# Kernel tuning notes

Measured on AMD Instinct MI355X. Metric: run time of the kernel, lower is better.

The kernel has to match this reference:

```python
import jax, jax.numpy as jnp
import numpy as np

N = 33_554_432  # 2^25 elements
N_CLASSES = 6


def setup_inputs() -> dict:
    key = jax.random.key(0)
    k1, k2 = jax.random.split(key)
    inputs = jax.random.normal(k1, (N,), dtype=jnp.float32)
    # targets are integer class labels stored as float32 (as torch l1_loss expects floats)
    targets = jax.random.randint(k2, (N,), 0, N_CLASSES).astype(jnp.float32)
    return {"inputs": inputs, "targets": targets}


def reference(inputs, targets):
    # Single-pass segment reduction replacing the per-class masked-gather loop.
    seg = targets.astype(jnp.int32)                      # class id per element
    absdiff = jnp.abs(inputs - targets)                  # |pred - target|
    sums = jax.ops.segment_sum(absdiff, seg, num_segments=N_CLASSES)
    counts = jax.ops.segment_sum(jnp.ones_like(absdiff), seg, num_segments=N_CLASSES)
    # Classes with zero members contribute 0 (the torch loop skips them).
    per_class_mae = jnp.where(counts > 0, sums / jnp.maximum(counts, 1.0), 0.0)
    return jnp.sum(per_class_mae) / N_CLASSES
```

## Files before the change

### kernel.cpp

```cpp
#include <hip/hip_runtime.h>

#define NCLASSES 6

__device__ __forceinline__ float wave_reduce_sum(float v) {
#pragma unroll
    for (int off = 32; off > 0; off >>= 1)
        v += __shfl_down(v, off, 64);
    return v;
}

__global__ void __launch_bounds__(256)
mae_partial_kernel(const float* __restrict__ inputs,
                   const float* __restrict__ targets,
                   float* __restrict__ partials,
                   int n) {
    float sums[NCLASSES] = {0.f, 0.f, 0.f, 0.f, 0.f, 0.f};
    float cnts[NCLASSES] = {0.f, 0.f, 0.f, 0.f, 0.f, 0.f};

    const int tid = blockIdx.x * blockDim.x + threadIdx.x;
    const int nthreads = gridDim.x * blockDim.x;
    const int n4 = n >> 2;

    const float4* __restrict__ in4 = reinterpret_cast<const float4*>(inputs);
    const float4* __restrict__ tg4 = reinterpret_cast<const float4*>(targets);

    for (int i = tid; i < n4; i += nthreads) {
        float4 x = in4[i];
        float4 t = tg4[i];

        float xs[4] = {x.x, x.y, x.z, x.w};
        float ts[4] = {t.x, t.y, t.z, t.w};
#pragma unroll
        for (int j = 0; j < 4; ++j) {
            float ad = fabsf(xs[j] - ts[j]);
#pragma unroll
            for (int k = 0; k < NCLASSES; ++k) {
                bool m = (ts[j] == (float)k);
                sums[k] += m ? ad : 0.f;
                cnts[k] += m ? 1.f : 0.f;
            }
        }
    }

    const int tail_start = n4 << 2;
    for (int i = tail_start + tid; i < n; i += nthreads) {
        float t = targets[i];
        float ad = fabsf(inputs[i] - t);
#pragma unroll
        for (int k = 0; k < NCLASSES; ++k) {
            bool m = (t == (float)k);
            sums[k] += m ? ad : 0.f;
            cnts[k] += m ? 1.f : 0.f;
        }
    }

    __shared__ float lds[4][12];
    const int lane = threadIdx.x & 63;
    const int wave = threadIdx.x >> 6;

#pragma unroll
    for (int k = 0; k < NCLASSES; ++k) {
        float s = wave_reduce_sum(sums[k]);
        float c = wave_reduce_sum(cnts[k]);
        if (lane == 0) {
            lds[wave][k] = s;
            lds[wave][k + NCLASSES] = c;
        }
    }
    __syncthreads();

    if (threadIdx.x < 12) {
        float v = lds[0][threadIdx.x] + lds[1][threadIdx.x] +
                  lds[2][threadIdx.x] + lds[3][threadIdx.x];
        partials[blockIdx.x * 12 + threadIdx.x] = v;
    }
}

__global__ void __launch_bounds__(256)
mae_finalize_kernel(const float* __restrict__ partials, int nblocks,
                    float* __restrict__ out) {
    float acc[12];
#pragma unroll
    for (int k = 0; k < 12; ++k) acc[k] = 0.f;

    for (int b = threadIdx.x; b < nblocks; b += blockDim.x) {
#pragma unroll
        for (int k = 0; k < 12; ++k) acc[k] += partials[b * 12 + k];
    }

    __shared__ float lds[4][12];
    const int lane = threadIdx.x & 63;
    const int wave = threadIdx.x >> 6;

#pragma unroll
    for (int k = 0; k < 12; ++k) {
        float v = wave_reduce_sum(acc[k]);
        if (lane == 0) lds[wave][k] = v;
    }
    __syncthreads();

    if (threadIdx.x == 0) {
        float total = 0.f;
#pragma unroll
        for (int c = 0; c < NCLASSES; ++c) {
            float s = lds[0][c] + lds[1][c] + lds[2][c] + lds[3][c];
            float n = lds[0][c + NCLASSES] + lds[1][c + NCLASSES] +
                      lds[2][c + NCLASSES] + lds[3][c + NCLASSES];
            total += (n > 0.f) ? (s / n) : 0.f;
        }
        out[0] = total / (float)NCLASSES;
    }
}

extern "C" void kernel_launch(void* const* d_in, const int* in_sizes, int n_in,
                              void* d_out, int out_size, void* d_ws, size_t ws_size,
                              hipStream_t stream) {
    const float* inputs  = (const float*)d_in[0];
    const float* targets = (const float*)d_in[1];
    float* out = (float*)d_out;
    float* partials = (float*)d_ws;

    const int n = in_sizes[0];
    const int NB = 2048;

    mae_partial_kernel<<<NB, 256, 0, stream>>>(inputs, targets, partials, n);
    mae_finalize_kernel<<<1, 256, 0, stream>>>(partials, NB, out);
}
```

Baseline: 54.01 us.

## Pack per-class counts into a 64-bit integer and unroll loads by four

Per-class float counters are replaced by one 64-bit packed integer, with a 10-bit field per class that is incremented by a shift. This cuts the per-element compare and select work. The main loop is also unrolled to issue four float4 loads per array before computing, which raises memory-level parallelism. Each thread handles at most 16 elements with 2048x256 threads, so the 10-bit fields will not overflow for this size. Larger inputs or per-thread counts above 1023 would corrupt the counts, and non-integer or out-of-range labels would misbehave.

New measurement: 57.15 us. 1.06x slower.

```diff
diff --git a/kernel.cpp b/kernel.cpp
--- a/kernel.cpp
+++ b/kernel.cpp
@@ -9,13 +9,29 @@
     return v;
 }
 
+__device__ __forceinline__ void process4(float4 x, float4 t,
+                                         float* __restrict__ sums,
+                                         unsigned long long& cpack) {
+    float xs[4] = {x.x, x.y, x.z, x.w};
+    float ts[4] = {t.x, t.y, t.z, t.w};
+#pragma unroll
+    for (int j = 0; j < 4; ++j) {
+        float ad = fabsf(xs[j] - ts[j]);
+        int cls = (int)ts[j];
+        cpack += 1ull << (cls * 10);
+#pragma unroll
+        for (int k = 0; k < NCLASSES; ++k)
+            sums[k] += (ts[j] == (float)k) ? ad : 0.f;
+    }
+}
+
 __global__ void __launch_bounds__(256)
 mae_partial_kernel(const float* __restrict__ inputs,
                    const float* __restrict__ targets,
                    float* __restrict__ partials,
                    int n) {
     float sums[NCLASSES] = {0.f, 0.f, 0.f, 0.f, 0.f, 0.f};
-    float cnts[NCLASSES] = {0.f, 0.f, 0.f, 0.f, 0.f, 0.f};
+    unsigned long long cpack = 0ull;
 
     const int tid = blockIdx.x * blockDim.x + threadIdx.x;
     const int nthreads = gridDim.x * blockDim.x;
@@ -24,35 +40,39 @@
     const float4* __restrict__ in4 = reinterpret_cast<const float4*>(inputs);
     const float4* __restrict__ tg4 = reinterpret_cast<const float4*>(targets);
 
-    for (int i = tid; i < n4; i += nthreads) {
-        float4 x = in4[i];
-        float4 t = tg4[i];
+    int i = tid;
+    for (; i + 3 * nthreads < n4; i += 4 * nthreads) {
+        float4 x0 = in4[i];
+        float4 x1 = in4[i + nthreads];
+        float4 x2 = in4[i + 2 * nthreads];
+        float4 x3 = in4[i + 3 * nthreads];
+        float4 t0 = tg4[i];
+        float4 t1 = tg4[i + nthreads];
+        float4 t2 = tg4[i + 2 * nthreads];
+        float4 t3 = tg4[i + 3 * nthreads];
+        process4(x0, t0, sums, cpack);
+        process4(x1, t1, sums, cpack);
+        process4(x2, t2, sums, cpack);
+        process4(x3, t3, sums, cpack);
+    }
+    for (; i < n4; i += nthreads)
+        process4(in4[i], tg4[i], sums, cpack);
 
-        float xs[4] = {x.x, x.y, x.z, x.w};
-        float ts[4] = {t.x, t.y, t.z, t.w};
+    const int tail_start = n4 << 2;
+    for (int s = tail_start + tid; s < n; s += nthreads) {
+        float t = targets[s];
+        float ad = fabsf(inputs[s] - t);
+        int cls = (int)t;
+        cpack += 1ull << (cls * 10);
 #pragma unroll
-        for (int j = 0; j < 4; ++j) {
-            float ad = fabsf(xs[j] - ts[j]);
-#pragma unroll
-            for (int k = 0; k < NCLASSES; ++k) {
-                bool m = (ts[j] == (float)k);
-                sums[k] += m ? ad : 0.f;
-                cnts[k] += m ? 1.f : 0.f;
-            }
-        }
+        for (int k = 0; k < NCLASSES; ++k)
+            sums[k] += (t == (float)k) ? ad : 0.f;
     }
 
-    const int tail_start = n4 << 2;
-    for (int i = tail_start + tid; i < n; i += nthreads) {
-        float t = targets[i];
-        float ad = fabsf(inputs[i] - t);
+    float cnts[NCLASSES];
 #pragma unroll
-        for (int k = 0; k < NCLASSES; ++k) {
-            bool m = (t == (float)k);
-            sums[k] += m ? ad : 0.f;
-            cnts[k] += m ? 1.f : 0.f;
-        }
-    }
+    for (int k = 0; k < NCLASSES; ++k)
+        cnts[k] = (float)((cpack >> (10 * k)) & 1023ull);
 
     __shared__ float lds[4][12];
     const int lane = threadIdx.x & 63;
```
